# Kernel tuning notes

Measured on AMD Instinct MI355X. Metric: run time of the kernel, lower is better.

Reference implementation:

```python
import jax, jax.numpy as jnp
import numpy as np

ALPHA = 0.2   # LeakyReLU negative slope
NEG = -9e15   # mask fill value from the torch code


def _conv1d(x, w, b):
    # x: (N, C_in, L), w: (C_out, C_in, 5), padding=2 -> same length
    y = jax.lax.conv_general_dilated(x, w, window_strides=(1,), padding=[(2, 2)],
                                     dimension_numbers=('NCH', 'OIH', 'NCH'))
    return y + b[None, :, None]


def _gat(h, mask, W, a):
    # Faithful to a_input @ a: e_ij = leakyrelu(Wh_i . a[:H] + Wh_j . a[H:])
    Wh = jnp.einsum('bnf,fo->bno', h, W)          # (B,N,H)
    H = W.shape[1]
    f1 = Wh @ a[:H]                               # (B,N,1)
    f2 = Wh @ a[H:]                               # (B,N,1)
    e = f1 + jnp.swapaxes(f2, 1, 2)               # (B,N,N)
    e = jnp.where(e > 0, e, ALPHA * e)            # LeakyReLU
    e = jnp.where(mask, e, NEG)
    att = jax.nn.softmax(e, axis=-1)              # dropout skipped (eval mode)
    return jnp.einsum('bij,bjo->bio', att, Wh)


def setup_inputs() -> dict:
    key = jax.random.key(0)
    ks = jax.random.split(key, 14)
    B, S, N, H, E = 8, 200, 512, 64, 2048
    sc = 0.1
    return {
        'x': jax.random.normal(ks[0], (B, S, N * 2), dtype=jnp.float32),
        'adj': jax.random.randint(ks[1], (N, N), 0, 2, dtype=jnp.int32),
        'edge_index': jax.random.randint(ks[2], (E, 2), 0, N, dtype=jnp.int32),
        'conv1_w': jax.random.normal(ks[3], (H // 2, 2, 5), dtype=jnp.float32) * sc,
        'conv1_b': jnp.zeros((H // 2,), dtype=jnp.float32),
        'conv2_w': jax.random.normal(ks[4], (H, H // 2, 5), dtype=jnp.float32) * sc,
        'conv2_b': jnp.zeros((H,), dtype=jnp.float32),
        'W1': jax.random.normal(ks[5], (H, H), dtype=jnp.float32) * sc,
        'a1': jax.random.normal(ks[6], (2 * H, 1), dtype=jnp.float32) * sc,
        'W2': jax.random.normal(ks[7], (H, H), dtype=jnp.float32) * sc,
        'a2': jax.random.normal(ks[8], (2 * H, 1), dtype=jnp.float32) * sc,
        'fc1_w': jax.random.normal(ks[9], (2 * H, H), dtype=jnp.float32) * sc,
        'fc1_b': jnp.zeros((H,), dtype=jnp.float32),
        'fc2_w': jax.random.normal(ks[10], (H, 1), dtype=jnp.float32) * sc,
        'fc2_b': jnp.zeros((1,), dtype=jnp.float32),
    }


def reference(x, adj, edge_index, conv1_w, conv1_b, conv2_w, conv2_b,
              W1, a1, W2, a2, fc1_w, fc1_b, fc2_w, fc2_b):
    B = x.shape[0]
    N = adj.shape[0]
    # (B,S,2N) -> (B,N,S,2) -> (B*N,2,S)
    xn = x.reshape(B, -1, N, 2).transpose(0, 2, 1, 3)
    xf = xn.reshape(B * N, -1, 2).transpose(0, 2, 1)
    h = jax.nn.relu(_conv1d(xf, conv1_w, conv1_b))
    h = jax.nn.relu(_conv1d(h, conv2_w, conv2_b))
    h = h.mean(axis=-1)                 # AdaptiveAvgPool1d(1) + squeeze
    h = h.reshape(B, N, -1)             # (B,N,H)
    mask = (adj > 0)[None]              # (1,N,N) broadcasts over batch
    h = jax.nn.relu(_gat(h, mask, W1, a1))
    h = _gat(h, mask, W2, a2)
    h1 = h[:, edge_index[:, 0]]         # (B,E,H)
    h2 = h[:, edge_index[:, 1]]
    he = jnp.concatenate([h1, h2], axis=-1)  # (B,E,2H)
    z = jax.nn.relu(he @ fc1_w + fc1_b)
    return jax.nn.sigmoid(z @ fc2_w + fc2_b).squeeze(-1)  # (B,E)
```

## Files before the change

kernel.cpp:

```cpp
#include <hip/hip_runtime.h>
#include <hip/hip_bf16.h>

typedef unsigned short u16;
typedef __attribute__((ext_vector_type(8))) short short8;
typedef __attribute__((ext_vector_type(4))) float float4v;
typedef __attribute__((ext_vector_type(16))) float float16v;

#define BATCH 8
#define SLEN  200
#define NNODE 512
#define C1    32
#define C2    64
#define NEDGE 2048
#define NEGV  -9000000000000000.0f

#define H1S 40
#define H1R 232
#define A1S 40

__device__ __forceinline__ u16 f2bf(float f) {
    unsigned int x = __float_as_uint(f);
    unsigned int lsb = (x >> 16) & 1u;
    x += 0x7fffu + lsb;
    return (u16)(x >> 16);
}

__device__ __forceinline__ float bf2f(u16 u) {
    return __uint_as_float(((unsigned int)u) << 16);
}

__device__ __forceinline__ unsigned int pk2(float a, float b) {
    __hip_bfloat162 h = __float22bfloat162_rn(make_float2(a, b));
    unsigned int r;
    __builtin_memcpy(&r, &h, 4);
    return r;
}

__global__ __launch_bounds__(256) void transpose_kernel(
    const float* __restrict__ x,
    float* __restrict__ xT)
{
    __shared__ float tile[32][33];
    const int t   = threadIdx.x;
    const int nc0 = blockIdx.x * 32;
    const int s0  = blockIdx.y * 32;
    const int b   = blockIdx.z;
    const int c   = t & 31, rr = t >> 5;

    #pragma unroll
    for (int r = 0; r < 4; ++r) {
        const int s = s0 + rr + r * 8;
        if (s < SLEN)
            tile[rr + r * 8][c] = x[((size_t)(b * SLEN + s)) * 1024 + nc0 + c];
    }
    __syncthreads();
    #pragma unroll
    for (int r = 0; r < 4; ++r) {
        const int nc = nc0 + rr + r * 8;
        const int s = s0 + c;
        if (s < SLEN)
            xT[((size_t)(b * 1024 + nc)) * SLEN + s] = tile[c][rr + r * 8];
    }
}

__global__ __launch_bounds__(256) void prep_kernel(
    const float* __restrict__ w1,
    const float* __restrict__ w2,
    u16* __restrict__ w1f,
    u16* __restrict__ w2f)
{
    const int t = threadIdx.x;
    if (t < 128) {
        const int nt = t >> 6;
        const int l  = t & 63;
        const int mml = l & 15, qq = l >> 4;
        const int oc = nt * 16 + mml;
        #pragma unroll
        for (int j = 0; j < 8; ++j) {
            const int k = qq * 8 + j;
            u16 val = 0;
            if (k < 10) {
                val = f2bf(w1[oc * 10 + k]);
            } else if (k < 20) {
                val = f2bf(w1[oc * 10 + (k - 10)]);
            } else if (k < 30) {
                const float wf = w1[oc * 10 + (k - 20)];
                val = f2bf(wf - bf2f(f2bf(wf)));
            }
            w1f[(nt * 64 + l) * 8 + j] = val;
        }
    }
    const int lane = t & 63, wv = t >> 6;
    if (wv == 0) {
        const int l31 = lane & 31, h = lane >> 5;
        #pragma unroll
        for (int kk = 0; kk < 5; ++kk)
            #pragma unroll
            for (int kc = 0; kc < 2; ++kc)
                #pragma unroll
                for (int nt = 0; nt < 2; ++nt) {
                    const int fid = (kk * 2 + kc) * 2 + nt;
                    const int oc  = nt * 32 + l31;
                    #pragma unroll
                    for (int j = 0; j < 8; ++j) {
                        const int c  = kc * 16 + h * 8 + j;
                        const int ic = (c & 1) * 16 + (c >> 1);
                        w2f[(fid * 64 + lane) * 8 + j] =
                            f2bf(w2[(size_t)oc * 160 + ic * 5 + kk]);
                    }
                }
    }
}

__global__ __launch_bounds__(256) void conv_fused_kernel(
    const float* __restrict__ xT,
    const float* __restrict__ b1,
    const float* __restrict__ b2,
    const float* __restrict__ W1,
    const float* __restrict__ a1,
    const u16* __restrict__ w1f,
    const u16* __restrict__ w2f,
    u16* __restrict__ Wh_bt,
    float* __restrict__ f1,
    float* __restrict__ f2)
{
    __shared__ unsigned int xhl[2][212];
    __shared__ __align__(16) u16 A1[208 * A1S];
    __shared__ __align__(16) u16 h1p[H1R * H1S];
    __shared__ float red[4][64];
    __shared__ float hm[64];
    __shared__ float part[4][64];

    const int t    = threadIdx.x;
    const int blk  = blockIdx.x;
    const int b    = blk >> 9;
    const int n    = blk & 511;
    const int lane = t & 63;
    const int wv   = t >> 6;
    const int ml   = lane & 15;
    const int q    = lane >> 4;
    const int l31  = lane & 31;
    const int h    = lane >> 5;

    const short8 w1frag0 = *(const short8*)(w1f + lane * 8);
    const short8 w1frag1 = *(const short8*)(w1f + (64 + lane) * 8);
    short8 wf[20];
    #pragma unroll
    for (int fid = 0; fid < 20; ++fid)
        wf[fid] = *(const short8*)(w2f + (fid * 64 + lane) * 8);
    const float bias1a = b1[ml];
    const float bias1b = b1[16 + ml];
    const float bias2a = b2[l31];
    const float bias2b = b2[32 + l31];

    if (t < SLEN) {
        const float x0 = xT[((size_t)(b * 1024 + 2 * n)) * SLEN + t];
        const float x1 = xT[((size_t)(b * 1024 + 2 * n + 1)) * SLEN + t];
        const u16 hx = f2bf(x0), hy = f2bf(x1);
        const u16 lx = f2bf(x0 - bf2f(hx));
        const u16 ly = f2bf(x1 - bf2f(hy));
        xhl[0][2 + t] = (unsigned int)hx | ((unsigned int)lx << 16);
        xhl[1][2 + t] = (unsigned int)hy | ((unsigned int)ly << 16);
    } else if (t < 212) {
        const int p = (t < 202) ? (t - 200) : t;
        xhl[0][p] = 0u;
        xhl[1][p] = 0u;
    }
    {
        unsigned int* hz = (unsigned int*)h1p;
        for (int idx = t; idx < 640; idx += 256)
            hz[(idx < 40) ? idx : (4000 + idx)] = 0u;
    }
    __syncthreads();

    if (t < 208) {
        unsigned int X0[5], X1[5];
        #pragma unroll
        for (int kk = 0; kk < 5; ++kk) {
            X0[kk] = xhl[0][t + kk];
            X1[kk] = xhl[1][t + kk];
        }
        unsigned int d[16];
        d[0] = (X0[0] & 0xffffu) | (X0[1] << 16);
        d[1] = (X0[2] & 0xffffu) | (X0[3] << 16);
        d[2] = (X0[4] & 0xffffu) | (X1[0] << 16);
        d[3] = (X1[1] & 0xffffu) | (X1[2] << 16);
        d[4] = (X1[3] & 0xffffu) | (X1[4] << 16);
        d[5] = (X0[0] >> 16) | (X0[1] & 0xffff0000u);
        d[6] = (X0[2] >> 16) | (X0[3] & 0xffff0000u);
        d[7] = (X0[4] >> 16) | (X1[0] & 0xffff0000u);
        d[8] = (X1[1] >> 16) | (X1[2] & 0xffff0000u);
        d[9] = (X1[3] >> 16) | (X1[4] & 0xffff0000u);
        d[10] = d[0]; d[11] = d[1]; d[12] = d[2]; d[13] = d[3]; d[14] = d[4];
        d[15] = 0u;
        unsigned int* row = (unsigned int*)&A1[t * A1S];
        #pragma unroll
        for (int ch = 0; ch < 4; ++ch)
            *(uint4*)(row + ch * 4) = make_uint4(d[ch*4], d[ch*4+1], d[ch*4+2], d[ch*4+3]);
    }
    __syncthreads();

    for (int mt = wv; mt < 13; mt += 4) {
        const short8 a = *(const short8*)&A1[(mt * 16 + ml) * A1S + q * 8];
        float4v c0 = {0.f, 0.f, 0.f, 0.f};
        float4v c1 = {0.f, 0.f, 0.f, 0.f};
        c0 = __builtin_amdgcn_mfma_f32_16x16x32_bf16(a, w1frag0, c0, 0, 0, 0);
        c1 = __builtin_amdgcn_mfma_f32_16x16x32_bf16(a, w1frag1, c1, 0, 0, 0);
        #pragma unroll
        for (int r = 0; r < 4; ++r) {
            const int m = mt * 16 + q * 4 + r;
            if (m < SLEN) {
                *(unsigned int*)&h1p[(2 + m) * H1S + 2 * ml] =
                    pk2(fmaxf(c0[r] + bias1a, 0.f), fmaxf(c1[r] + bias1b, 0.f));
            }
        }
    }
    __syncthreads();

    float total0 = 0.f, total1 = 0.f;
    for (int mt = wv; mt < 7; mt += 4) {
        const int m0 = mt * 32;
        float16v acc0 = {0.f,0.f,0.f,0.f,0.f,0.f,0.f,0.f,0.f,0.f,0.f,0.f,0.f,0.f,0.f,0.f};
        float16v acc1 = {0.f,0.f,0.f,0.f,0.f,0.f,0.f,0.f,0.f,0.f,0.f,0.f,0.f,0.f,0.f,0.f};
        #pragma unroll
        for (int kk = 0; kk < 5; ++kk) {
            #pragma unroll
            for (int kc = 0; kc < 2; ++kc) {
                const short8 a = *(const short8*)
                    &h1p[(2 + m0 + l31 + kk) * H1S + kc * 16 + h * 8];
                acc0 = __builtin_amdgcn_mfma_f32_32x32x16_bf16(a, wf[(kk*2+kc)*2+0], acc0, 0, 0, 0);
                acc1 = __builtin_amdgcn_mfma_f32_32x32x16_bf16(a, wf[(kk*2+kc)*2+1], acc1, 0, 0, 0);
            }
        }
        if (mt < 6) {
            #pragma unroll
            for (int reg = 0; reg < 16; ++reg) {
                total0 += fmaxf(acc0[reg] + bias2a, 0.f);
                total1 += fmaxf(acc1[reg] + bias2b, 0.f);
            }
        } else {
            #pragma unroll
            for (int reg = 0; reg < 4; ++reg) {
                total0 += fmaxf(acc0[reg] + bias2a, 0.f);
                total1 += fmaxf(acc1[reg] + bias2b, 0.f);
            }
        }
    }
    total0 += __shfl_xor(total0, 32, 64);
    total1 += __shfl_xor(total1, 32, 64);
    if (lane < 32) {
        red[wv][l31]      = total0;
        red[wv][32 + l31] = total1;
    }
    __syncthreads();
    if (t < 64)
        hm[t] = (red[0][t] + red[1][t] + red[2][t] + red[3][t]) * (1.0f / 200.0f);
    __syncthreads();

    {
        const int o = t & 63, q4 = t >> 6;
        const float* Wp = W1 + (q4 * 16) * 64 + o;
        float p = 0.f;
        #pragma unroll
        for (int k = 0; k < 16; ++k) p += hm[q4 * 16 + k] * Wp[k * 64];
        part[q4][o] = p;
    }
    __syncthreads();
    if (t < 64) {
        const float v = part[0][t] + part[1][t] + part[2][t] + part[3][t];
        Wh_bt[((size_t)(b * 64 + t)) * 512 + n] = f2bf(v);
        float v1 = v * a1[t];
        float v2 = v * a1[64 + t];
        #pragma unroll
        for (int off = 32; off; off >>= 1) {
            v1 += __shfl_xor(v1, off, 64);
            v2 += __shfl_xor(v2, off, 64);
        }
        if (t == 0) { f1[b * 512 + n] = v1; f2[b * 512 + n] = v2; }
    }
}

__global__ __launch_bounds__(256) void gat_wh_kernel(
    const float* __restrict__ h,
    const float* __restrict__ W,
    const float* __restrict__ a,
    u16* __restrict__ Wh_bt,
    float* __restrict__ f1,
    float* __restrict__ f2)
{
    __shared__ __align__(16) u16 hA[64 * 72];
    __shared__ __align__(16) u16 Wt[64 * 72];
    __shared__ __align__(16) u16 whT[64 * 72];
    __shared__ float as[128];

    const int t    = threadIdx.x;
    const int blk  = blockIdx.x;
    const int b    = blk >> 3;
    const int j0   = (blk & 7) * 64;
    const int lane = t & 63, wv = t >> 6, ml = lane & 15, q = lane >> 4;

    {
        const int r = t >> 2, c0 = (t & 3) * 16;
        const float* hp = h + ((size_t)(b * 512 + j0 + r)) * 64 + c0;
        #pragma unroll
        for (int v = 0; v < 4; ++v) {
            float4 f = *(const float4*)(hp + v * 4);
            unsigned int* dst = (unsigned int*)&hA[r * 72 + c0 + v * 4];
            dst[0] = pk2(f.x, f.y);
            dst[1] = pk2(f.z, f.w);
        }
    }
    {
        const int k = t >> 2, o0 = (t & 3) * 16;
        const float* wp = W + k * 64 + o0;
        #pragma unroll
        for (int v = 0; v < 16; ++v)
            Wt[(o0 + v) * 72 + k] = f2bf(wp[v]);
    }
    if (t < 128) as[t] = a[t];
    __syncthreads();

    short8 af0 = *(const short8*)&hA[(16 * wv + ml) * 72 + q * 8];
    short8 af1 = *(const short8*)&hA[(16 * wv + ml) * 72 + 32 + q * 8];
    float4v acc[4];
    #pragma unroll
    for (int nt = 0; nt < 4; ++nt) {
        short8 b0 = *(const short8*)&Wt[(16 * nt + ml) * 72 + q * 8];
        short8 b1 = *(const short8*)&Wt[(16 * nt + ml) * 72 + 32 + q * 8];
        float4v c = {0.f, 0.f, 0.f, 0.f};
        c = __builtin_amdgcn_mfma_f32_16x16x32_bf16(af0, b0, c, 0, 0, 0);
        c = __builtin_amdgcn_mfma_f32_16x16x32_bf16(af1, b1, c, 0, 0, 0);
        acc[nt] = c;
    }

    #pragma unroll
    for (int nt = 0; nt < 4; ++nt) {
        unsigned int* dst = (unsigned int*)&whT[(16 * nt + ml) * 72 + 16 * wv + q * 4];
        dst[0] = pk2(acc[nt][0], acc[nt][1]);
        dst[1] = pk2(acc[nt][2], acc[nt][3]);
    }

    #pragma unroll
    for (int r = 0; r < 4; ++r) {
        float v1 = 0.f, v2 = 0.f;
        #pragma unroll
        for (int nt = 0; nt < 4; ++nt) {
            const float w = acc[nt][r];
            v1 += w * as[16 * nt + ml];
            v2 += w * as[64 + 16 * nt + ml];
        }
        v1 += __shfl_xor(v1, 1, 64); v2 += __shfl_xor(v2, 1, 64);
        v1 += __shfl_xor(v1, 2, 64); v2 += __shfl_xor(v2, 2, 64);
        v1 += __shfl_xor(v1, 4, 64); v2 += __shfl_xor(v2, 4, 64);
        v1 += __shfl_xor(v1, 8, 64); v2 += __shfl_xor(v2, 8, 64);
        if (ml == 0) {
            const int j = j0 + 16 * wv + q * 4 + r;
            f1[b * 512 + j] = v1;
            f2[b * 512 + j] = v2;
        }
    }
    __syncthreads();

    {
        const int o = t >> 2, js = (t & 3) * 16;
        u16* dst = Wh_bt + ((size_t)(b * 64 + o)) * 512 + j0 + js;
        *(short8*)dst = *(const short8*)&whT[o * 72 + js];
    }
}

#define PSTR 520
__global__ __launch_bounds__(512) void gat_attn_kernel(
    const u16* __restrict__ Wh_bt,
    const float* __restrict__ f1,
    const float* __restrict__ f2,
    const int* __restrict__ adj,
    float* __restrict__ outp,
    const int do_relu)
{
    __shared__ __align__(16) u16 P[16 * PSTR];
    __shared__ float f2s[512];
    __shared__ float invs[16];
    __shared__ float f1s[16];
    __shared__ float accH[4][64][4];

    const int t   = threadIdx.x;
    const int blk = blockIdx.x;
    const int b   = blk >> 5;
    const int i0  = (blk & 31) * 16;

    f2s[t & 511] = f2[b * 512 + (t & 511)];
    if (t < 16) f1s[t] = f1[b * 512 + i0 + t];
    __syncthreads();

    {
        const int i = t >> 5, jseg = t & 31;
        const float f1i = f1s[i];
        const int* arow = adj + (size_t)(i0 + i) * 512 + jseg * 16;
        const float* f2p = f2s + jseg * 16;
        float ev[16];
        float mx = -3.0e38f;
        #pragma unroll
        for (int v = 0; v < 4; ++v) {
            const int4 a4 = *(const int4*)(arow + v * 4);
            #pragma unroll
            for (int u = 0; u < 4; ++u) {
                const int msk = (&a4.x)[u];
                float e = f1i + f2p[v * 4 + u];
                e = e > 0.f ? e : 0.2f * e;
                e = (msk > 0) ? e : NEGV;
                ev[v * 4 + u] = e;
                mx = fmaxf(mx, e);
            }
        }
        mx = fmaxf(mx, __shfl_xor(mx, 1, 64));
        mx = fmaxf(mx, __shfl_xor(mx, 2, 64));
        mx = fmaxf(mx, __shfl_xor(mx, 4, 64));
        mx = fmaxf(mx, __shfl_xor(mx, 8, 64));
        mx = fmaxf(mx, __shfl_xor(mx, 16, 64));
        float sum = 0.f;
        #pragma unroll
        for (int v = 0; v < 16; ++v) {
            const float ex = __expf(ev[v] - mx);
            ev[v] = ex;
            sum += ex;
        }
        sum += __shfl_xor(sum, 1, 64);
        sum += __shfl_xor(sum, 2, 64);
        sum += __shfl_xor(sum, 4, 64);
        sum += __shfl_xor(sum, 8, 64);
        sum += __shfl_xor(sum, 16, 64);
        if (jseg == 0) invs[i] = 1.0f / sum;
        unsigned int* prow = (unsigned int*)&P[i * PSTR + jseg * 16];
        #pragma unroll
        for (int v = 0; v < 8; ++v)
            prow[v] = pk2(ev[2 * v], ev[2 * v + 1]);
    }
    __syncthreads();

    const int lane = t & 63, wv = t >> 6, nt = wv & 3, kh = wv >> 2;
    const int ml = lane & 15, q = lane >> 4;
    const u16* Bp = Wh_bt + ((size_t)(b * 64 + nt * 16 + ml)) * 512 + kh * 256 + q * 8;
    float4v acc = {0.f, 0.f, 0.f, 0.f};
    #pragma unroll
    for (int ks = 0; ks < 8; ++ks) {
        const short8 afr = *(const short8*)&P[ml * PSTR + kh * 256 + ks * 32 + q * 8];
        const short8 bfr = *(const short8*)(Bp + ks * 32);
        acc = __builtin_amdgcn_mfma_f32_16x16x32_bf16(afr, bfr, acc, 0, 0, 0);
    }
    if (kh == 1) {
        #pragma unroll
        for (int r = 0; r < 4; ++r) accH[nt][lane][r] = acc[r];
    }
    __syncthreads();
    if (kh == 0) {
        #pragma unroll
        for (int r = 0; r < 4; ++r) {
            const int i2 = q * 4 + r;
            float val = (acc[r] + accH[nt][lane][r]) * invs[i2];
            if (do_relu) val = fmaxf(val, 0.f);
            outp[((size_t)(b * 512 + i0 + i2)) * 64 + nt * 16 + ml] = val;
        }
    }
}

#define FSTR 136
__global__ __launch_bounds__(256) void edge_mlp_kernel(
    const float* __restrict__ hg,
    const int* __restrict__ eidx,
    const float* __restrict__ fc1w,
    const float* __restrict__ fc1b,
    const float* __restrict__ fc2w,
    const float* __restrict__ fc2b,
    float* __restrict__ out)
{
    __shared__ __align__(16) u16 fwT[64 * FSTR];
    __shared__ __align__(16) u16 he[16 * FSTR];
    __shared__ float part[16][4];
    __shared__ float b1s[64], w2s[64];

    const int t   = threadIdx.x;
    const int blk = blockIdx.x;
    const int b   = blk >> 7;
    const int e0  = (blk & 127) * 16;

    {
        const int k = t >> 1, o0 = (t & 1) * 32;
        const float* wp = fc1w + k * 64 + o0;
        #pragma unroll
        for (int v = 0; v < 32; ++v)
            fwT[(o0 + v) * FSTR + k] = f2bf(wp[v]);
    }
    if (t < 64) { b1s[t] = fc1b[t]; w2s[t] = fc2w[t]; }
    {
        const int ep = t >> 4, p = t & 15;
        const int e = e0 + ep;
        const int node = (p < 8) ? eidx[e * 2] : eidx[e * 2 + 1];
        const int c0 = (p & 7) * 8;
        const float* hp = hg + ((size_t)(b * 512 + node)) * 64 + c0;
        const float4 fa = *(const float4*)hp;
        const float4 fb = *(const float4*)(hp + 4);
        unsigned int* dst = (unsigned int*)&he[ep * FSTR + ((p < 8) ? 0 : 64) + c0];
        dst[0] = pk2(fa.x, fa.y);
        dst[1] = pk2(fa.z, fa.w);
        dst[2] = pk2(fb.x, fb.y);
        dst[3] = pk2(fb.z, fb.w);
    }
    __syncthreads();

    const int lane = t & 63, wv = t >> 6, ml = lane & 15, q = lane >> 4;
    float4v acc = {0.f, 0.f, 0.f, 0.f};
    #pragma unroll
    for (int ks = 0; ks < 4; ++ks) {
        const short8 afr = *(const short8*)&he[ml * FSTR + ks * 32 + q * 8];
        const short8 bfr = *(const short8*)&fwT[(16 * wv + ml) * FSTR + ks * 32 + q * 8];
        acc = __builtin_amdgcn_mfma_f32_16x16x32_bf16(afr, bfr, acc, 0, 0, 0);
    }
    const int o = 16 * wv + ml;
    const float bo = b1s[o], wo = w2s[o];
    #pragma unroll
    for (int r = 0; r < 4; ++r) {
        float z = fmaxf(acc[r] + bo, 0.f) * wo;
        z += __shfl_xor(z, 1, 64);
        z += __shfl_xor(z, 2, 64);
        z += __shfl_xor(z, 4, 64);
        z += __shfl_xor(z, 8, 64);
        if (ml == 0) part[q * 4 + r][wv] = z;
    }
    __syncthreads();
    if (t < 16) {
        const float v = part[t][0] + part[t][1] + part[t][2] + part[t][3] + fc2b[0];
        out[b * 2048 + e0 + t] = 1.0f / (1.0f + __expf(-v));
    }
}

extern "C" void kernel_launch(void* const* d_in, const int* in_sizes, int n_in,
                              void* d_out, int out_size, void* d_ws, size_t ws_size,
                              hipStream_t stream) {
    const float* x    = (const float*)d_in[0];
    const int* adj    = (const int*)d_in[1];
    const int* eidx   = (const int*)d_in[2];
    const float* w1   = (const float*)d_in[3];
    const float* b1   = (const float*)d_in[4];
    const float* w2   = (const float*)d_in[5];
    const float* b2   = (const float*)d_in[6];
    const float* W1   = (const float*)d_in[7];
    const float* a1   = (const float*)d_in[8];
    const float* W2   = (const float*)d_in[9];
    const float* a2   = (const float*)d_in[10];
    const float* fc1w = (const float*)d_in[11];
    const float* fc1b = (const float*)d_in[12];
    const float* fc2w = (const float*)d_in[13];
    const float* fc2b = (const float*)d_in[14];
    float* out = (float*)d_out;

    float* ws = (float*)d_ws;
    const size_t R = (size_t)BATCH * NNODE;
    float* g    = ws;
    float* f1   = g + R * 64;
    float* f2   = f1 + R;
    u16*   whbt = (u16*)(f2 + R);
    u16*   w1f  = whbt + R * 64;
    u16*   w2f  = w1f + 1024;
    float* xT   = (float*)(w2f + 10240);

    transpose_kernel<<<dim3(32, 7, 8), dim3(256), 0, stream>>>(x, xT);
    prep_kernel<<<dim3(1), dim3(256), 0, stream>>>(w1, w2, w1f, w2f);
    conv_fused_kernel<<<dim3(R), dim3(256), 0, stream>>>(
        xT, b1, b2, W1, a1, w1f, w2f, whbt, f1, f2);
    gat_attn_kernel<<<dim3(256), dim3(512), 0, stream>>>(whbt, f1, f2, adj, g, 1);
    gat_wh_kernel<<<dim3(64), dim3(256), 0, stream>>>(g, W2, a2, whbt, f1, f2);
    gat_attn_kernel<<<dim3(256), dim3(512), 0, stream>>>(whbt, f1, f2, adj, g, 0);
    edge_mlp_kernel<<<dim3(1024), dim3(256), 0, stream>>>(
        g, eidx, fc1w, fc1b, fc2w, fc2b, out);
}
```

Measured before the change: 152.6 us.

## Merge transpose and weight prep, process two nodes per conv block, prepack fc1

Folds the transpose and the weight-prep kernels into one launch, where the last block also packs the fc1 weights into bf16 MFMA fragments. The edge MLP then loads these prepacked fragments into registers instead of converting and transposing fc1 through shared memory in every block. The fused conv kernel now handles two nodes per block, so the per-block register loading of the conv2 weight fragments and the W1 projection reads are amortised over twice the work. The cost is more shared memory per conv block and fewer blocks, which may lower occupancy.

```diff
diff --git a/kernel.cpp b/kernel.cpp
--- a/kernel.cpp
+++ b/kernel.cpp
@@ -9,8 +9,6 @@
 #define BATCH 8
 #define SLEN  200
 #define NNODE 512
-#define C1    32
-#define C2    64
 #define NEDGE 2048
 #define NEGV  -9000000000000000.0f
 
@@ -36,40 +34,49 @@
     return r;
 }
 
-__global__ __launch_bounds__(256) void transpose_kernel(
+__global__ __launch_bounds__(256) void pre_kernel(
     const float* __restrict__ x,
-    float* __restrict__ xT)
+    const float* __restrict__ w1,
+    const float* __restrict__ w2,
+    const float* __restrict__ fc1w,
+    float* __restrict__ xT,
+    u16* __restrict__ w1f,
+    u16* __restrict__ w2f,
+    u16* __restrict__ efw)
 {
     __shared__ float tile[32][33];
-    const int t   = threadIdx.x;
-    const int nc0 = blockIdx.x * 32;
-    const int s0  = blockIdx.y * 32;
-    const int b   = blockIdx.z;
-    const int c   = t & 31, rr = t >> 5;
-
-    #pragma unroll
-    for (int r = 0; r < 4; ++r) {
-        const int s = s0 + rr + r * 8;
-        if (s < SLEN)
-            tile[rr + r * 8][c] = x[((size_t)(b * SLEN + s)) * 1024 + nc0 + c];
-    }
-    __syncthreads();
-    #pragma unroll
-    for (int r = 0; r < 4; ++r) {
-        const int nc = nc0 + rr + r * 8;
-        const int s = s0 + c;
-        if (s < SLEN)
-            xT[((size_t)(b * 1024 + nc)) * SLEN + s] = tile[c][rr + r * 8];
-    }
-}
-
-__global__ __launch_bounds__(256) void prep_kernel(
-    const float* __restrict__ w1,
-    const float* __restrict__ w2,
-    u16* __restrict__ w1f,
-    u16* __restrict__ w2f)
-{
     const int t = threadIdx.x;
+    const int blk = blockIdx.x;
+
+    if (blk < 1792) {
+        const int xi  = blk & 31;
+        const int rem = blk >> 5;
+        const int yi  = rem % 7;
+        const int zi  = rem / 7;
+        const int nc0 = xi * 32;
+        const int s0  = yi * 32;
+        const int c   = t & 31, rr = t >> 5;
+        #pragma unroll
+        for (int r = 0; r < 4; ++r) {
+            const int s = s0 + rr + r * 8;
+            if (s < SLEN)
+                tile[rr + r * 8][c] = x[((size_t)(zi * SLEN + s)) * 1024 + nc0 + c];
+        }
+        __syncthreads();
+        #pragma unroll
+        for (int r = 0; r < 4; ++r) {
+            const int nc = nc0 + rr + r * 8;
+            const int s = s0 + c;
+            if (s < SLEN)
+                xT[((size_t)(zi * 1024 + nc)) * SLEN + s] = tile[c][rr + r * 8];
+        }
+        return;
+    }
+
+    const int lane = t & 63, wv = t >> 6;
+    const int ml = lane & 15, q = lane >> 4;
+    const int l31 = lane & 31, h = lane >> 5;
+
     if (t < 128) {
         const int nt = t >> 6;
         const int l  = t & 63;
@@ -90,25 +97,24 @@
             w1f[(nt * 64 + l) * 8 + j] = val;
         }
     }
-    const int lane = t & 63, wv = t >> 6;
-    if (wv == 0) {
-        const int l31 = lane & 31, h = lane >> 5;
-        #pragma unroll
-        for (int kk = 0; kk < 5; ++kk)
-            #pragma unroll
-            for (int kc = 0; kc < 2; ++kc)
-                #pragma unroll
-                for (int nt = 0; nt < 2; ++nt) {
-                    const int fid = (kk * 2 + kc) * 2 + nt;
-                    const int oc  = nt * 32 + l31;
-                    #pragma unroll
-                    for (int j = 0; j < 8; ++j) {
-                        const int c  = kc * 16 + h * 8 + j;
-                        const int ic = (c & 1) * 16 + (c >> 1);
-                        w2f[(fid * 64 + lane) * 8 + j] =
-                            f2bf(w2[(size_t)oc * 160 + ic * 5 + kk]);
-                    }
-                }
+    for (int fid = wv; fid < 20; fid += 4) {
+        const int kk = fid >> 2, kc = (fid >> 1) & 1, nt = fid & 1;
+        const int oc = nt * 32 + l31;
+        #pragma unroll
+        for (int j = 0; j < 8; ++j) {
+            const int c  = kc * 16 + h * 8 + j;
+            const int ic = (c & 1) * 16 + (c >> 1);
+            w2f[(fid * 64 + lane) * 8 + j] = f2bf(w2[(size_t)oc * 160 + ic * 5 + kk]);
+        }
+    }
+    for (int u = wv; u < 16; u += 4) {
+        const int ks = u >> 2, wvv = u & 3;
+        const int o = wvv * 16 + ml;
+        #pragma unroll
+        for (int j = 0; j < 8; ++j) {
+            const int k = ks * 32 + q * 8 + j;
+            efw[(u * 64 + lane) * 8 + j] = f2bf(fc1w[k * 64 + o]);
+        }
     }
 }
 
@@ -124,17 +130,18 @@
     float* __restrict__ f1,
     float* __restrict__ f2)
 {
-    __shared__ unsigned int xhl[2][212];
+    __shared__ unsigned int xhl[2][2][212];
     __shared__ __align__(16) u16 A1[208 * A1S];
-    __shared__ __align__(16) u16 h1p[H1R * H1S];
-    __shared__ float red[4][64];
-    __shared__ float hm[64];
-    __shared__ float part[4][64];
+    __shared__ __align__(16) u16 h1p[2 * H1R * H1S];
+    __shared__ float red[4][2][64];
+    __shared__ float hm[2][64];
+    __shared__ float part[2][4][64];
 
     const int t    = threadIdx.x;
     const int blk  = blockIdx.x;
-    const int b    = blk >> 9;
-    const int n    = blk & 511;
+    const int b    = blk >> 8;
+    const int pair = blk & 255;
+    const int n0   = pair * 2;
     const int lane = t & 63;
     const int wv   = t >> 6;
     const int ml   = lane & 15;
@@ -154,72 +161,81 @@
     const float bias2b = b2[32 + l31];
 
     if (t < SLEN) {
-        const float x0 = xT[((size_t)(b * 1024 + 2 * n)) * SLEN + t];
-        const float x1 = xT[((size_t)(b * 1024 + 2 * n + 1)) * SLEN + t];
-        const u16 hx = f2bf(x0), hy = f2bf(x1);
-        const u16 lx = f2bf(x0 - bf2f(hx));
-        const u16 ly = f2bf(x1 - bf2f(hy));
-        xhl[0][2 + t] = (unsigned int)hx | ((unsigned int)lx << 16);
-        xhl[1][2 + t] = (unsigned int)hy | ((unsigned int)ly << 16);
+        const float* xp = xT + ((size_t)(b * 1024 + 4 * pair)) * SLEN + t;
+        #pragma unroll
+        for (int u = 0; u < 4; ++u) {
+            const float xv = xp[u * SLEN];
+            const u16 hi = f2bf(xv);
+            const u16 lo = f2bf(xv - bf2f(hi));
+            xhl[u >> 1][u & 1][2 + t] = (unsigned int)hi | ((unsigned int)lo << 16);
+        }
     } else if (t < 212) {
         const int p = (t < 202) ? (t - 200) : t;
-        xhl[0][p] = 0u;
-        xhl[1][p] = 0u;
+        xhl[0][0][p] = 0u; xhl[0][1][p] = 0u;
+        xhl[1][0][p] = 0u; xhl[1][1][p] = 0u;
     }
     {
         unsigned int* hz = (unsigned int*)h1p;
-        for (int idx = t; idx < 640; idx += 256)
-            hz[(idx < 40) ? idx : (4000 + idx)] = 0u;
-    }
-    __syncthreads();
-
-    if (t < 208) {
-        unsigned int X0[5], X1[5];
-        #pragma unroll
-        for (int kk = 0; kk < 5; ++kk) {
-            X0[kk] = xhl[0][t + kk];
-            X1[kk] = xhl[1][t + kk];
-        }
-        unsigned int d[16];
-        d[0] = (X0[0] & 0xffffu) | (X0[1] << 16);
-        d[1] = (X0[2] & 0xffffu) | (X0[3] << 16);
-        d[2] = (X0[4] & 0xffffu) | (X1[0] << 16);
-        d[3] = (X1[1] & 0xffffu) | (X1[2] << 16);
-        d[4] = (X1[3] & 0xffffu) | (X1[4] << 16);
-        d[5] = (X0[0] >> 16) | (X0[1] & 0xffff0000u);
-        d[6] = (X0[2] >> 16) | (X0[3] & 0xffff0000u);
-        d[7] = (X0[4] >> 16) | (X1[0] & 0xffff0000u);
-        d[8] = (X1[1] >> 16) | (X1[2] & 0xffff0000u);
-        d[9] = (X1[3] >> 16) | (X1[4] & 0xffff0000u);
-        d[10] = d[0]; d[11] = d[1]; d[12] = d[2]; d[13] = d[3]; d[14] = d[4];
-        d[15] = 0u;
-        unsigned int* row = (unsigned int*)&A1[t * A1S];
-        #pragma unroll
-        for (int ch = 0; ch < 4; ++ch)
-            *(uint4*)(row + ch * 4) = make_uint4(d[ch*4], d[ch*4+1], d[ch*4+2], d[ch*4+3]);
-    }
-    __syncthreads();
-
-    for (int mt = wv; mt < 13; mt += 4) {
-        const short8 a = *(const short8*)&A1[(mt * 16 + ml) * A1S + q * 8];
-        float4v c0 = {0.f, 0.f, 0.f, 0.f};
-        float4v c1 = {0.f, 0.f, 0.f, 0.f};
-        c0 = __builtin_amdgcn_mfma_f32_16x16x32_bf16(a, w1frag0, c0, 0, 0, 0);
-        c1 = __builtin_amdgcn_mfma_f32_16x16x32_bf16(a, w1frag1, c1, 0, 0, 0);
-        #pragma unroll
-        for (int r = 0; r < 4; ++r) {
-            const int m = mt * 16 + q * 4 + r;
-            if (m < SLEN) {
-                *(unsigned int*)&h1p[(2 + m) * H1S + 2 * ml] =
-                    pk2(fmaxf(c0[r] + bias1a, 0.f), fmaxf(c1[r] + bias1b, 0.f));
+        for (int idx = t; idx < 1280; idx += 256) {
+            const int nd = idx >= 640;
+            const int i2 = idx - nd * 640;
+            hz[nd * 4640 + ((i2 < 40) ? i2 : (4000 + i2))] = 0u;
+        }
+    }
+    __syncthreads();
+
+    for (int nd = 0; nd < 2; ++nd) {
+        if (t < 208) {
+            unsigned int X0[5], X1[5];
+            #pragma unroll
+            for (int kk = 0; kk < 5; ++kk) {
+                X0[kk] = xhl[nd][0][t + kk];
+                X1[kk] = xhl[nd][1][t + kk];
             }
-        }
-    }
-    __syncthreads();
-
-    float total0 = 0.f, total1 = 0.f;
-    for (int mt = wv; mt < 7; mt += 4) {
+            unsigned int d[16];
+            d[0] = (X0[0] & 0xffffu) | (X0[1] << 16);
+            d[1] = (X0[2] & 0xffffu) | (X0[3] << 16);
+            d[2] = (X0[4] & 0xffffu) | (X1[0] << 16);
+            d[3] = (X1[1] & 0xffffu) | (X1[2] << 16);
+            d[4] = (X1[3] & 0xffffu) | (X1[4] << 16);
+            d[5] = (X0[0] >> 16) | (X0[1] & 0xffff0000u);
+            d[6] = (X0[2] >> 16) | (X0[3] & 0xffff0000u);
+            d[7] = (X0[4] >> 16) | (X1[0] & 0xffff0000u);
+            d[8] = (X1[1] >> 16) | (X1[2] & 0xffff0000u);
+            d[9] = (X1[3] >> 16) | (X1[4] & 0xffff0000u);
+            d[10] = d[0]; d[11] = d[1]; d[12] = d[2]; d[13] = d[3]; d[14] = d[4];
+            d[15] = 0u;
+            unsigned int* row = (unsigned int*)&A1[t * A1S];
+            #pragma unroll
+            for (int ch = 0; ch < 4; ++ch)
+                *(uint4*)(row + ch * 4) = make_uint4(d[ch*4], d[ch*4+1], d[ch*4+2], d[ch*4+3]);
+        }
+        __syncthreads();
+
+        for (int mt = wv; mt < 13; mt += 4) {
+            const short8 a = *(const short8*)&A1[(mt * 16 + ml) * A1S + q * 8];
+            float4v c0 = {0.f, 0.f, 0.f, 0.f};
+            float4v c1 = {0.f, 0.f, 0.f, 0.f};
+            c0 = __builtin_amdgcn_mfma_f32_16x16x32_bf16(a, w1frag0, c0, 0, 0, 0);
+            c1 = __builtin_amdgcn_mfma_f32_16x16x32_bf16(a, w1frag1, c1, 0, 0, 0);
+            #pragma unroll
+            for (int r = 0; r < 4; ++r) {
+                const int m = mt * 16 + q * 4 + r;
+                if (m < SLEN) {
+                    *(unsigned int*)&h1p[(nd * H1R + 2 + m) * H1S + 2 * ml] =
+                        pk2(fmaxf(c0[r] + bias1a, 0.f), fmaxf(c1[r] + bias1b, 0.f));
+                }
+            }
+        }
+        __syncthreads();
+    }
+
+    float tot00 = 0.f, tot01 = 0.f, tot10 = 0.f, tot11 = 0.f;
+    for (int tile = wv; tile < 14; tile += 4) {
+        const int nd = (tile >= 7);
+        const int mt = nd ? (tile - 7) : tile;
         const int m0 = mt * 32;
+        const int rbase = nd * H1R + m0 + l31;
         float16v acc0 = {0.f,0.f,0.f,0.f,0.f,0.f,0.f,0.f,0.f,0.f,0.f,0.f,0.f,0.f,0.f,0.f};
         float16v acc1 = {0.f,0.f,0.f,0.f,0.f,0.f,0.f,0.f,0.f,0.f,0.f,0.f,0.f,0.f,0.f,0.f};
         #pragma unroll
@@ -227,56 +243,73 @@
             #pragma unroll
             for (int kc = 0; kc < 2; ++kc) {
                 const short8 a = *(const short8*)
-                    &h1p[(2 + m0 + l31 + kk) * H1S + kc * 16 + h * 8];
+                    &h1p[(rbase + kk) * H1S + kc * 16 + h * 8];
                 acc0 = __builtin_amdgcn_mfma_f32_32x32x16_bf16(a, wf[(kk*2+kc)*2+0], acc0, 0, 0, 0);
                 acc1 = __builtin_amdgcn_mfma_f32_32x32x16_bf16(a, wf[(kk*2+kc)*2+1], acc1, 0, 0, 0);
             }
         }
+        float s0 = 0.f, s1 = 0.f;
         if (mt < 6) {
             #pragma unroll
             for (int reg = 0; reg < 16; ++reg) {
-                total0 += fmaxf(acc0[reg] + bias2a, 0.f);
-                total1 += fmaxf(acc1[reg] + bias2b, 0.f);
+                s0 += fmaxf(acc0[reg] + bias2a, 0.f);
+                s1 += fmaxf(acc1[reg] + bias2b, 0.f);
             }
         } else {
             #pragma unroll
             for (int reg = 0; reg < 4; ++reg) {
-                total0 += fmaxf(acc0[reg] + bias2a, 0.f);
-                total1 += fmaxf(acc1[reg] + bias2b, 0.f);
+                s0 += fmaxf(acc0[reg] + bias2a, 0.f);
+                s1 += fmaxf(acc1[reg] + bias2b, 0.f);
             }
         }
-    }
-    total0 += __shfl_xor(total0, 32, 64);
-    total1 += __shfl_xor(total1, 32, 64);
+        if (nd == 0) { tot00 += s0; tot01 += s1; }
+        else         { tot10 += s0; tot11 += s1; }
+    }
+    tot00 += __shfl_xor(tot00, 32, 64);
+    tot01 += __shfl_xor(tot01, 32, 64);
+    tot10 += __shfl_xor(tot10, 32, 64);
+    tot11 += __shfl_xor(tot11, 32, 64);
     if (lane < 32) {
-        red[wv][l31]      = total0;
-        red[wv][32 + l31] = total1;
-    }
-    __syncthreads();
-    if (t < 64)
-        hm[t] = (red[0][t] + red[1][t] + red[2][t] + red[3][t]) * (1.0f / 200.0f);
+        red[wv][0][l31]      = tot00;
+        red[wv][0][32 + l31] = tot01;
+        red[wv][1][l31]      = tot10;
+        red[wv][1][32 + l31] = tot11;
+    }
+    __syncthreads();
+    if (t < 128) {
+        const int nd = t >> 6, o = t & 63;
+        hm[nd][o] = (red[0][nd][o] + red[1][nd][o] + red[2][nd][o] + red[3][nd][o])
+                    * (1.0f / 200.0f);
+    }
     __syncthreads();
 
     {
         const int o = t & 63, q4 = t >> 6;
         const float* Wp = W1 + (q4 * 16) * 64 + o;
-        float p = 0.f;
-        #pragma unroll
-        for (int k = 0; k < 16; ++k) p += hm[q4 * 16 + k] * Wp[k * 64];
-        part[q4][o] = p;
-    }
-    __syncthreads();
-    if (t < 64) {
-        const float v = part[0][t] + part[1][t] + part[2][t] + part[3][t];
-        Wh_bt[((size_t)(b * 64 + t)) * 512 + n] = f2bf(v);
-        float v1 = v * a1[t];
-        float v2 = v * a1[64 + t];
+        float p0 = 0.f, p1 = 0.f;
+        #pragma unroll
+        for (int k = 0; k < 16; ++k) {
+            const float w = Wp[k * 64];
+            p0 += hm[0][q4 * 16 + k] * w;
+            p1 += hm[1][q4 * 16 + k] * w;
+        }
+        part[0][q4][o] = p0;
+        part[1][q4][o] = p1;
+    }
+    __syncthreads();
+    if (t < 128) {
+        const int nd = t >> 6, o = t & 63;
+        const int n = n0 + nd;
+        const float v = part[nd][0][o] + part[nd][1][o] + part[nd][2][o] + part[nd][3][o];
+        Wh_bt[((size_t)(b * 64 + o)) * 512 + n] = f2bf(v);
+        float v1 = v * a1[o];
+        float v2 = v * a1[64 + o];
         #pragma unroll
         for (int off = 32; off; off >>= 1) {
             v1 += __shfl_xor(v1, off, 64);
             v2 += __shfl_xor(v2, off, 64);
         }
-        if (t == 0) { f1[b * 512 + n] = v1; f2[b * 512 + n] = v2; }
+        if (o == 0) { f1[b * 512 + n] = v1; f2[b * 512 + n] = v2; }
     }
 }
 
@@ -467,30 +500,29 @@
 __global__ __launch_bounds__(256) void edge_mlp_kernel(
     const float* __restrict__ hg,
     const int* __restrict__ eidx,
-    const float* __restrict__ fc1w,
+    const u16* __restrict__ efw,
     const float* __restrict__ fc1b,
     const float* __restrict__ fc2w,
     const float* __restrict__ fc2b,
     float* __restrict__ out)
 {
-    __shared__ __align__(16) u16 fwT[64 * FSTR];
     __shared__ __align__(16) u16 he[16 * FSTR];
     __shared__ float part[16][4];
-    __shared__ float b1s[64], w2s[64];
 
     const int t   = threadIdx.x;
     const int blk = blockIdx.x;
     const int b   = blk >> 7;
     const int e0  = (blk & 127) * 16;
-
-    {
-        const int k = t >> 1, o0 = (t & 1) * 32;
-        const float* wp = fc1w + k * 64 + o0;
-        #pragma unroll
-        for (int v = 0; v < 32; ++v)
-            fwT[(o0 + v) * FSTR + k] = f2bf(wp[v]);
-    }
-    if (t < 64) { b1s[t] = fc1b[t]; w2s[t] = fc2w[t]; }
+    const int lane = t & 63, wv = t >> 6, ml = lane & 15, q = lane >> 4;
+
+    short8 bw[4];
+    #pragma unroll
+    for (int ks = 0; ks < 4; ++ks)
+        bw[ks] = *(const short8*)(efw + ((ks * 4 + wv) * 64 + lane) * 8);
+    const int o = 16 * wv + ml;
+    const float bo = fc1b[o];
+    const float wo = fc2w[o];
+
     {
         const int ep = t >> 4, p = t & 15;
         const int e = e0 + ep;
@@ -507,16 +539,12 @@
     }
     __syncthreads();
 
-    const int lane = t & 63, wv = t >> 6, ml = lane & 15, q = lane >> 4;
     float4v acc = {0.f, 0.f, 0.f, 0.f};
     #pragma unroll
     for (int ks = 0; ks < 4; ++ks) {
         const short8 afr = *(const short8*)&he[ml * FSTR + ks * 32 + q * 8];
-        const short8 bfr = *(const short8*)&fwT[(16 * wv + ml) * FSTR + ks * 32 + q * 8];
-        acc = __builtin_amdgcn_mfma_f32_16x16x32_bf16(afr, bfr, acc, 0, 0, 0);
-    }
-    const int o = 16 * wv + ml;
-    const float bo = b1s[o], wo = w2s[o];
+        acc = __builtin_amdgcn_mfma_f32_16x16x32_bf16(afr, bw[ks], acc, 0, 0, 0);
+    }
     #pragma unroll
     for (int r = 0; r < 4; ++r) {
         float z = fmaxf(acc[r] + bo, 0.f) * wo;
@@ -561,15 +589,15 @@
     u16*   whbt = (u16*)(f2 + R);
     u16*   w1f  = whbt + R * 64;
     u16*   w2f  = w1f + 1024;
-    float* xT   = (float*)(w2f + 10240);
-
-    transpose_kernel<<<dim3(32, 7, 8), dim3(256), 0, stream>>>(x, xT);
-    prep_kernel<<<dim3(1), dim3(256), 0, stream>>>(w1, w2, w1f, w2f);
-    conv_fused_kernel<<<dim3(R), dim3(256), 0, stream>>>(
+    u16*   efw  = w2f + 10240;
+    float* xT   = (float*)(efw + 8192);
+
+    pre_kernel<<<dim3(1793), dim3(256), 0, stream>>>(x, w1, w2, fc1w, xT, w1f, w2f, efw);
+    conv_fused_kernel<<<dim3(2048), dim3(256), 0, stream>>>(
         xT, b1, b2, W1, a1, w1f, w2f, whbt, f1, f2);
     gat_attn_kernel<<<dim3(256), dim3(512), 0, stream>>>(whbt, f1, f2, adj, g, 1);
     gat_wh_kernel<<<dim3(64), dim3(256), 0, stream>>>(g, W2, a2, whbt, f1, f2);
     gat_attn_kernel<<<dim3(256), dim3(512), 0, stream>>>(whbt, f1, f2, adj, g, 0);
     edge_mlp_kernel<<<dim3(1024), dim3(256), 0, stream>>>(
-        g, eidx, fc1w, fc1b, fc2w, fc2b, out);
-}
+        g, eidx, efw, fc1b, fc2w, fc2b, out);
+}
```

New measurement: 151.4 us. No clear change (-0.8%).
